# Performance work log

Hardware: AMD Instinct MI355X
Metric: run time of the kernel (lower is better)

## Reference

```python
import jax, jax.numpy as jnp
import numpy as np

K = 5        # spline kernel_size per dim (dim=2 -> 25 kernel weights)
NPG = 75     # MNIST superpixel nodes per graph


def _spline_conv(x, src, dst, pseudo, emask, W, root, bias):
    """SplineConv, dim=2, kernel_size=5, degree=1 open splines, aggr='mean'.
    emask in {0,1} masks out coalesced-away (duplicate/self-loop) edges."""
    n = x.shape[0]
    v = jnp.clip(pseudo, 0.0, 1.0) * (K - 1)
    bot = jnp.clip(jnp.floor(v), 0, K - 2)
    frac = v - bot                                   # [E,2]
    bot = bot.astype(jnp.int32)
    xj = x[src] * emask[:, None]                     # [E,Fin] gathered source feats
    # aggregate-then-transform: acc[k,i,:] = sum over edges into i with basis k
    acc = jnp.zeros((K * K, n, x.shape[1]), x.dtype)
    for o0 in (0, 1):
        for o1 in (0, 1):
            w = (frac[:, 0] if o0 else 1.0 - frac[:, 0]) * (frac[:, 1] if o1 else 1.0 - frac[:, 1])
            kk = (bot[:, 0] + o0) + K * (bot[:, 1] + o1)
            acc = acc.at[kk, dst].add(w[:, None] * xj)
    out = jnp.einsum('knf,kfo->no', acc, W)
    deg = jax.ops.segment_sum(emask, dst, num_segments=n)
    return out / jnp.maximum(deg, 1.0)[:, None] + x @ root + bias


def _pool(x, pos, valid, batch, src, dst, emask, size, G, B):
    """voxel_grid + max_pool with static shapes: S=B*G*G clusters, masked."""
    S = B * G * G
    c = jnp.clip(jnp.floor(pos / size).astype(jnp.int32), 0, G - 1)
    cl = batch * (G * G) + c[:, 1] * G + c[:, 0]
    xm = jnp.where(valid[:, None] > 0, x, -1e30)
    px = jax.ops.segment_max(xm, cl, num_segments=S)
    cnt = jax.ops.segment_sum(valid, cl, num_segments=S)
    sval = (cnt > 0).astype(x.dtype)
    px = jnp.where(sval[:, None] > 0, px, 0.0)
    ppos = jax.ops.segment_sum(pos * valid[:, None], cl, num_segments=S) / jnp.maximum(cnt, 1.0)[:, None]
    nb = jnp.arange(S, dtype=jnp.int32) // (G * G)
    # remap edges to clusters; mask self loops and duplicates (= coalesce)
    nsrc, ndst = cl[src], cl[dst]
    m = (emask > 0) & (nsrc != ndst)
    a0 = jnp.where(m, nsrc, S)
    b0 = jnp.where(m, ndst, S)
    order = jnp.lexsort((b0, a0))
    a, b = a0[order], b0[order]
    first = jnp.concatenate([jnp.array([True]), (a[1:] != a[:-1]) | (b[1:] != b[:-1])])
    keep = jnp.zeros(src.shape[0], dtype=bool).at[order].set(first & (a < S))
    kf = keep.astype(x.dtype)
    # T.Cartesian(cat=False, norm=True): pseudo = (pos_src-pos_dst)/(2*max|.|)+0.5
    cart = ppos[nsrc] - ppos[ndst]
    amax = jnp.maximum(jnp.max(jnp.abs(cart) * kf[:, None]), 1e-12)
    pseudo = cart / (2.0 * amax) + 0.5
    return px, ppos, sval, nb, nsrc, ndst, kf, pseudo


def _forward(x, pos, src, dst, W1, r1, b1, W2, r2, b2, W3, r3, b3, fw1, fb1, fw2, fb2):
    N = x.shape[0]
    B = N // NPG
    batch = jnp.arange(N, dtype=jnp.int32) // NPG
    valid = jnp.ones((N,), x.dtype)
    emask = jnp.ones((src.shape[0],), x.dtype)
    cart = pos[src] - pos[dst]
    pseudo = cart / (2.0 * jnp.maximum(jnp.max(jnp.abs(cart)), 1e-12)) + 0.5
    x = jax.nn.elu(_spline_conv(x, src, dst, pseudo, emask, W1, r1, b1))
    x, pos, valid, batch, src, dst, emask, pseudo = _pool(x, pos, valid, batch, src, dst, emask, 5.0, 6, B)
    x = jax.nn.elu(_spline_conv(x, src, dst, pseudo, emask, W2, r2, b2))
    x, pos, valid, batch, src, dst, emask, pseudo = _pool(x, pos, valid, batch, src, dst, emask, 7.0, 5, B)
    x = jax.nn.elu(_spline_conv(x, src, dst, pseudo, emask, W3, r3, b3))
    # max_pool_x(cluster, x, batch, size=4): 2x2 voxel grid (size=14, end=27.99)
    c = jnp.clip(jnp.floor(pos / 14.0).astype(jnp.int32), 0, 1)
    cl = batch * 4 + c[:, 1] * 2 + c[:, 0]
    xm = jnp.where(valid[:, None] > 0, x, -1e30)
    px = jax.ops.segment_max(xm, cl, num_segments=B * 4)
    cnt = jax.ops.segment_sum(valid, cl, num_segments=B * 4)
    px = jnp.where((cnt > 0)[:, None], px, 0.0)
    h = jax.nn.elu(px.reshape(B, 4 * 64) @ fw1.T + fb1)
    logits = h @ fw2.T + fb2  # F.dropout is identity in eval mode
    return jax.nn.log_softmax(logits, axis=1)


def setup_inputs() -> dict:
    key = jax.random.key(0)
    ks = jax.random.split(key, 16)
    B, EPG = 1024, 1392
    N = B * NPG
    x = jax.random.normal(ks[0], (N, 1), jnp.float32)
    pos = jax.random.uniform(ks[1], (N, 2), jnp.float32) * 27.99
    s = jax.random.randint(ks[2], (B, EPG), 0, NPG)
    d = (s + 1 + jax.random.randint(ks[3], (B, EPG), 0, NPG - 1)) % NPG  # no self loops
    off = (jnp.arange(B, dtype=jnp.int32) * NPG)[:, None]
    src = (s + off).reshape(-1)
    dst = (d + off).reshape(-1)
    rn = lambda k, sh, sc: jax.random.normal(k, sh, jnp.float32) * sc
    return dict(x=x, pos=pos, src=src, dst=dst,
                W1=rn(ks[4], (25, 1, 32), 0.2), r1=rn(ks[5], (1, 32), 0.2), b1=jnp.zeros((32,), jnp.float32),
                W2=rn(ks[6], (25, 32, 64), 0.05), r2=rn(ks[7], (32, 64), 0.1), b2=jnp.zeros((64,), jnp.float32),
                W3=rn(ks[8], (25, 64, 64), 0.04), r3=rn(ks[9], (64, 64), 0.08), b3=jnp.zeros((64,), jnp.float32),
                fw1=rn(ks[10], (128, 256), 0.06), fb1=jnp.zeros((128,), jnp.float32),
                fw2=rn(ks[11], (10, 128), 0.09), fb2=jnp.zeros((10,), jnp.float32))


def reference(x, pos, src, dst, W1, r1, b1, W2, r2, b2, W3, r3, b3, fw1, fb1, fw2, fb2):
    return _forward(x, pos, src, dst, W1, r1, b1, W2, r2, b2, W3, r3, b3, fw1, fb1, fw2, fb2)
```

## Files before the change

kernel.cpp:

```cpp
#include <hip/hip_runtime.h>
#include <math.h>

#define NPG 75
#define KDIM 5

typedef _Float16 half8 __attribute__((ext_vector_type(8)));
typedef float f32x4 __attribute__((ext_vector_type(4)));

__device__ __forceinline__ float eluf(float v){ return v > 0.f ? v : expf(v) - 1.f; }

__device__ __forceinline__ void atomAddF(float* p, float v){ unsafeAtomicAdd(p, v); }

__device__ __forceinline__ unsigned fenc(float f){
    unsigned u = __float_as_uint(f);
    return (u & 0x80000000u) ? ~u : (u | 0x80000000u);
}
__device__ __forceinline__ float fdec(unsigned u){
    return (u & 0x80000000u) ? __uint_as_float(u & 0x7FFFFFFFu) : __uint_as_float(~u);
}

__device__ __forceinline__ void fma25(float (&r)[25], const float (&wx)[5], const float (&wyx)[5]){
    #pragma unroll
    for (int b1 = 0; b1 < 5; b1++)
        #pragma unroll
        for (int b0 = 0; b0 < 5; b0++)
            asm("v_fmac_f32 %0, %1, %2" : "+v"(r[b1 * 5 + b0]) : "v"(wx[b0]), "v"(wyx[b1]));
}

__device__ __forceinline__ void spline2(float c0, float c1, float am, int* kks, float* wsp){
    float denom = 2.f * fmaxf(am, 1e-12f);
    float p0 = c0 / denom + 0.5f;
    float p1 = c1 / denom + 0.5f;
    p0 = fminf(fmaxf(p0, 0.f), 1.f) * 4.f;
    p1 = fminf(fmaxf(p1, 0.f), 1.f) * 4.f;
    float b0 = fminf(floorf(p0), 3.f);
    float b1 = fminf(floorf(p1), 3.f);
    float f0 = p0 - b0, f1 = p1 - b1;
    int i0 = (int)b0, i1 = (int)b1;
    wsp[0] = (1.f - f0) * (1.f - f1); kks[0] = i0     + KDIM *  i1;
    wsp[1] =        f0  * (1.f - f1); kks[1] = i0 + 1 + KDIM *  i1;
    wsp[2] = (1.f - f0) *        f1 ; kks[2] = i0     + KDIM * (i1 + 1);
    wsp[3] =        f0  *        f1 ; kks[3] = i0 + 1 + KDIM * (i1 + 1);
}

__device__ __forceinline__ void spline_pay(float2 c, float denom, float* d){
    float p0 = fminf(fmaxf(c.x / denom + 0.5f, 0.f), 1.f) * 4.f;
    float p1 = fminf(fmaxf(c.y / denom + 0.5f, 0.f), 1.f) * 4.f;
    float b0 = fminf(floorf(p0), 3.f);
    float b1 = fminf(floorf(p1), 3.f);
    int i0 = (int)b0, i1 = (int)b1;
    float f0 = p0 - b0, f1 = p1 - b1;
    #pragma unroll
    for (int k = 0; k < 4; k++){
        d[k]     = (k == i0) ? (1.f - f0) : ((k == i0 + 1) ? f0 : 0.f);
        d[4 + k] = (k == i1) ? (1.f - f1) : ((k == i1 + 1) ? f1 : 0.f);
    }
}

__global__ __launch_bounds__(256) void prep_k(
        const float* __restrict__ W2, const float* __restrict__ r2,
        const float* __restrict__ W3, const float* __restrict__ r3,
        _Float16* __restrict__ Wz2, _Float16* __restrict__ Wz3, int nW,
        const float* __restrict__ pos, const int* __restrict__ src,
        const int* __restrict__ dst, int E4, int gA, unsigned* __restrict__ outbits){
    const int blk = blockIdx.x;
    if (blk < nW){
        int gid = blk * 256 + threadIdx.x;
        const int T2 = 26 * 32 * 64;
        const int T3 = 26 * 64 * 64;
        const float* W; const float* root; _Float16* Wz; int FIN; int g;
        if (gid < T2){ W = W2; root = r2; Wz = Wz2; FIN = 32; g = gid; }
        else if (gid < T2 + T3){ W = W3; root = r3; Wz = Wz3; FIN = 64; g = gid - T2; }
        else return;
        int k = g >> 6, n = g & 63;
        float v = (k < 25 * FIN) ? W[(size_t)k * 64 + n] : root[(size_t)(k - 25 * FIN) * 64 + n];
        int kt = k >> 5, kr = k & 31, quad = kr >> 3, j = kr & 7;
        int lane = (quad << 4) | (n & 15);
        int nt = n >> 4;
        Wz[(((size_t)(kt * 4 + nt) * 64 + lane) << 3) + j] = (_Float16)v;
    } else {
        float cand = 0.f;
        for (int i = (blk - nW) * 256 + threadIdx.x; i < E4; i += gA * 256){
            int4 s4 = ((const int4*)src)[i];
            int4 d4 = ((const int4*)dst)[i];
            #pragma unroll
            for (int k = 0; k < 4; k++){
                int s = (&s4.x)[k], d = (&d4.x)[k];
                float c0 = pos[s*2]   - pos[d*2];
                float c1 = pos[s*2+1] - pos[d*2+1];
                cand = fmaxf(cand, fmaxf(fabsf(c0), fabsf(c1)));
            }
        }
        __shared__ float sm[256];
        sm[threadIdx.x] = cand; __syncthreads();
        for (int o = 128; o > 0; o >>= 1){
            if (threadIdx.x < o) sm[threadIdx.x] = fmaxf(sm[threadIdx.x], sm[threadIdx.x + o]);
            __syncthreads();
        }
        if (threadIdx.x == 0) atomicMax(outbits, __float_as_uint(sm[0]));
    }
}

__global__ __launch_bounds__(512) void conv1dedup_k(
        const float* __restrict__ x, const float* __restrict__ pos,
        const int* __restrict__ src, const int* __restrict__ dst, int EPG,
        const unsigned* __restrict__ amaxp,
        const float* __restrict__ W1, const float* __restrict__ r1, const float* __restrict__ b1,
        float* __restrict__ px1, float* __restrict__ pp1, float* __restrict__ sv1,
        int* __restrict__ easrc, float2* __restrict__ ecart,
        int* __restrict__ rowptr2, int* __restrict__ kcnt, unsigned* __restrict__ amaxbits){
    __shared__ __align__(16) float acc[NPG * 28];
    __shared__ float deg[NPG];
    __shared__ float xl[NPG], p0l[NPG], p1l[NPG];
    __shared__ int   cli[NPG];
    __shared__ float W1s[800], r1s[32], b1s[32];
    __shared__ unsigned px[36 * 32];
    __shared__ float cnt[36], ps[72], ppS[72];
    __shared__ unsigned pm[36 * 36];
    __shared__ float degs[36];
    __shared__ int rs[37], cur[36];
    __shared__ float red[8];
    __shared__ unsigned short sdS[2048];

    const int b = blockIdx.x, t = threadIdx.x;
    const int lane = t & 63, wid = t >> 6;
    const int n0 = b * NPG, e0 = b * EPG;

    const float am = __uint_as_float(*amaxp);

    for (int i = t; i < NPG * 28; i += 512) acc[i] = 0.f;
    for (int i = t; i < 36 * 32; i += 512) px[i] = 0u;
    for (int i = t; i < 36 * 36; i += 512) pm[i] = 0xFFFFFFFFu;
    if (t < NPG) deg[t] = 0.f;
    if (t < 36){ cnt[t] = 0.f; degs[t] = 0.f; }
    if (t < 72) ps[t] = 0.f;
    for (int i = t; i < 800; i += 512) W1s[i] = W1[i];
    if (t < 32){ r1s[t] = r1[t]; b1s[t] = b1[t]; }
    if (t < NPG){
        float p0 = pos[(n0 + t) * 2], p1 = pos[(n0 + t) * 2 + 1];
        xl[t] = x[n0 + t]; p0l[t] = p0; p1l[t] = p1;
        int c0 = min(max((int)floorf(p0 / 5.f), 0), 5);
        int c1 = min(max((int)floorf(p1 / 5.f), 0), 5);
        cli[t] = c1 * 6 + c0;
    }
    __syncthreads();

    if (t < NPG){
        int c = cli[t];
        atomAddF(&cnt[c], 1.f);
        atomAddF(&ps[c*2],     p0l[t]);
        atomAddF(&ps[c*2 + 1], p1l[t]);
    }
    #pragma unroll 4
    for (int it = 0; it < 4; it++){
        int e = t + it * 512;
        if (e < EPG){
            int s = src[e0 + e] - n0;
            int d = dst[e0 + e] - n0;
            sdS[e] = (unsigned short)(s | (d << 8));
            float c0 = p0l[s] - p0l[d];
            float c1 = p1l[s] - p1l[d];
            int kks[4]; float wsp[4];
            spline2(c0, c1, am, kks, wsp);
            float xv = xl[s];
            #pragma unroll
            for (int c = 0; c < 4; c++) atomAddF(&acc[d*28 + kks[c]], wsp[c] * xv);
            atomAddF(&deg[d], 1.f);
        }
    }
    __syncthreads();

    if (t < 36){
        float c = cnt[t], m = fmaxf(c, 1.f);
        float q0 = ps[t*2] / m, q1 = ps[t*2 + 1] / m;
        ppS[t*2] = q0; ppS[t*2 + 1] = q1;
        pp1[(b*36 + t)*2]     = q0;
        pp1[(b*36 + t)*2 + 1] = q1;
        sv1[b*36 + t] = (c > 0.f) ? 1.f : 0.f;
    }
    {
        const int o = t & 31;
        float wreg[25];
        #pragma unroll
        for (int k = 0; k < 25; k++) wreg[k] = W1s[k * 32 + o];
        const float rro = r1s[o], bbo = b1s[o];
        const int ii = t >> 5;
        #pragma unroll
        for (int r = 0; r < 5; r++){
            int i = ii + r * 16;
            if (i < NPG){
                const float4* ar = (const float4*)(acc + i * 28);
                float s = 0.f;
                #pragma unroll
                for (int q = 0; q < 7; q++){
                    float4 aq = ar[q];
                    s += aq.x * wreg[q*4];
                    if (q*4 + 1 < 25) s += aq.y * wreg[q*4 + 1];
                    if (q*4 + 2 < 25) s += aq.z * wreg[q*4 + 2];
                    if (q*4 + 3 < 25) s += aq.w * wreg[q*4 + 3];
                }
                float v = s / fmaxf(deg[i], 1.f) + xl[i] * rro + bbo;
                v = eluf(v);
                atomicMax(&px[cli[i]*32 + o], fenc(v));
            }
        }
    }
    int lab[4];
    #pragma unroll 4
    for (int it = 0; it < 4; it++){
        int e = t + it * 512;
        lab[it] = 0;
        if (e < EPG){
            int sd = (int)sdS[e];
            int a  = cli[sd & 255];
            int bb = cli[sd >> 8];
            lab[it] = a | (bb << 8) | ((a != bb) ? 0x10000 : 0);
            if (a != bb) atomicMin(&pm[a * 36 + bb], (unsigned)e);
        }
    }
    __syncthreads();

    for (int idx = t; idx < 36 * 32; idx += 512){
        int s_ = idx >> 5;
        px1[(size_t)(b*36)*32 + idx] = (cnt[s_] > 0.f) ? fdec(px[idx]) : 0.f;
    }
    float cand = 0.f;
    unsigned keptM = 0;
    #pragma unroll 4
    for (int it = 0; it < 4; it++){
        int e = t + it * 512;
        int L = lab[it];
        if (L & 0x10000){
            int a = L & 255, bb = (L >> 8) & 255;
            if (pm[a * 36 + bb] == (unsigned)e){
                keptM |= 1u << it;
                atomAddF(&degs[bb], 1.f);
                float c0 = ppS[a*2]     - ppS[bb*2];
                float c1 = ppS[a*2 + 1] - ppS[bb*2 + 1];
                cand = fmaxf(cand, fmaxf(fabsf(c0), fabsf(c1)));
            }
        }
    }
    #pragma unroll
    for (int o = 1; o < 64; o <<= 1) cand = fmaxf(cand, __shfl_xor(cand, o, 64));
    if (lane == 0) red[wid] = cand;
    __syncthreads();
    if (t == 0){
        float m = red[0];
        #pragma unroll
        for (int i = 1; i < 8; i++) m = fmaxf(m, red[i]);
        atomicMax(amaxbits, __float_as_uint(m));
    }
    if (t < 64){
        int v = (t < 36) ? (int)degs[t] : 0;
        int incl = v;
        #pragma unroll
        for (int o = 1; o < 64; o <<= 1){
            int u = __shfl_up(incl, o, 64);
            if (t >= o) incl += u;
        }
        if (t == 0) rs[0] = 0;
        if (t < 36) rs[t + 1] = incl;
    }
    __syncthreads();
    if (t < 36){
        rowptr2[(b*36 + t)*2]     = e0 + rs[t];
        rowptr2[(b*36 + t)*2 + 1] = e0 + rs[t + 1];
        cur[t] = rs[t];
    }
    if (t == 0) kcnt[b] = rs[36];
    __syncthreads();
    #pragma unroll 4
    for (int it = 0; it < 4; it++){
        if (keptM & (1u << it)){
            int L = lab[it];
            int a = L & 255, bb = (L >> 8) & 255;
            int slot = atomicAdd(&cur[bb], 1);
            easrc[e0 + slot] = b*36 + a;
            ecart[e0 + slot] = make_float2(ppS[a*2] - ppS[bb*2], ppS[a*2 + 1] - ppS[bb*2 + 1]);
        }
    }
}

__global__ __launch_bounds__(1024) void dedup_pool_k(
        const int* __restrict__ easrc_in, const int* __restrict__ rowptr_in,
        const int* __restrict__ kcnt_in,
        const float* __restrict__ xin,
        const float* __restrict__ pp1, const float* __restrict__ sv1,
        int EPG,
        float* __restrict__ px2, float* __restrict__ pp2, float* __restrict__ sv2,
        int* __restrict__ easrc, float2* __restrict__ ecart,
        int* __restrict__ rowptr2, int* __restrict__ kcnt, unsigned* __restrict__ amaxbits){
    constexpr int GG = 25, NN = 36;
    __shared__ unsigned pm[GG * GG];
    __shared__ float degs[GG];
    __shared__ int rs[GG + 1];
    __shared__ int cur[GG];
    __shared__ float red[16];
    __shared__ int   clS[NN];
    __shared__ int   vld[NN];
    __shared__ int   rsS[NN + 1];
    __shared__ float ppS[2 * GG];
    __shared__ unsigned px[GG * 64];
    __shared__ float cnt[GG], ps[2 * GG];
    __shared__ unsigned short abS[1280];

    const int b = blockIdx.x, t = threadIdx.x;
    const int lane = t & 63, wid = t >> 6;
    const int e0 = b * EPG;
    const int cb25 = b * GG;
    const int nb36 = b * NN;

    for (int i = t; i < GG * GG; i += 1024) pm[i] = 0xFFFFFFFFu;
    for (int i = t; i < GG * 64; i += 1024) px[i] = 0u;
    if (t < GG){ degs[t] = 0.f; cnt[t] = 0.f; }
    if (t < 2 * GG) ps[t] = 0.f;
    if (t < NN){
        float v  = sv1[nb36 + t];
        float p0 = pp1[(nb36 + t)*2], p1 = pp1[(nb36 + t)*2 + 1];
        int c0 = min(max((int)floorf(p0 / 7.f), 0), 4);
        int c1 = min(max((int)floorf(p1 / 7.f), 0), 4);
        clS[t] = c1 * 5 + c0;
        vld[t] = (v > 0.f) ? 1 : 0;
        rsS[t] = rowptr_in[(nb36 + t)*2] - e0;
    }
    if (t == 0) rsS[NN] = kcnt_in[b];
    __syncthreads();

    const int kn = rsS[NN];

    if (t < NN && vld[t]){
        int c = clS[t];
        atomAddF(&cnt[c], 1.f);
        atomAddF(&ps[c*2],     pp1[(nb36 + t)*2]);
        atomAddF(&ps[c*2 + 1], pp1[(nb36 + t)*2 + 1]);
    }
    for (int idx = t; idx < NN * 64; idx += 1024){
        int i = idx >> 6, f = idx & 63;
        if (vld[i])
            atomicMax(&px[clS[i]*64 + f], fenc(xin[(size_t)(nb36 + i)*64 + f]));
    }
    #pragma unroll 2
    for (int it = 0; it < 2; it++){
        int s = t + it * 1024;
        if (s < kn){
            int r = 0;
            while (r < NN - 1 && rsS[r + 1] <= s) r++;
            int a2 = clS[easrc_in[e0 + s] - nb36];
            int b2 = clS[r];
            abS[s] = (unsigned short)(a2 | (b2 << 8) | ((a2 != b2) ? 0x8000 : 0));
            if (a2 != b2) atomicMin(&pm[a2 * GG + b2], (unsigned)s);
        }
    }
    __syncthreads();

    if (t < GG){
        float c = cnt[t], m = fmaxf(c, 1.f);
        float q0 = ps[t*2] / m, q1 = ps[t*2 + 1] / m;
        ppS[t*2] = q0; ppS[t*2 + 1] = q1;
        pp2[(cb25 + t)*2]     = q0;
        pp2[(cb25 + t)*2 + 1] = q1;
        sv2[cb25 + t] = (c > 0.f) ? 1.f : 0.f;
    }
    for (int idx = t; idx < GG * 64; idx += 1024){
        int s_ = idx >> 6;
        px2[(size_t)cb25*64 + idx] = (cnt[s_] > 0.f) ? fdec(px[idx]) : 0.f;
    }
    __syncthreads();

    float cand = 0.f;
    #pragma unroll 2
    for (int it = 0; it < 2; it++){
        int s = t + it * 1024;
        if (s < kn){
            int A = (int)abS[s];
            if (A & 0x8000){
                int a2 = A & 255, b2 = (A >> 8) & 127;
                if (pm[a2 * GG + b2] == (unsigned)s){
                    atomAddF(&degs[b2], 1.f);
                    float c0 = ppS[a2*2]     - ppS[b2*2];
                    float c1 = ppS[a2*2 + 1] - ppS[b2*2 + 1];
                    cand = fmaxf(cand, fmaxf(fabsf(c0), fabsf(c1)));
                }
            }
        }
    }
    #pragma unroll
    for (int o = 1; o < 64; o <<= 1) cand = fmaxf(cand, __shfl_xor(cand, o, 64));
    if (lane == 0) red[wid] = cand;
    __syncthreads();
    if (t == 0){
        float m = red[0];
        #pragma unroll
        for (int i = 1; i < 16; i++) m = fmaxf(m, red[i]);
        atomicMax(amaxbits, __float_as_uint(m));
    }
    if (t < 64){
        int v = (t < GG) ? (int)degs[t] : 0;
        int incl = v;
        #pragma unroll
        for (int o = 1; o < 64; o <<= 1){
            int u = __shfl_up(incl, o, 64);
            if (t >= o) incl += u;
        }
        if (t == 0) rs[0] = 0;
        if (t < GG) rs[t + 1] = incl;
    }
    __syncthreads();
    if (t < GG){
        rowptr2[(cb25 + t)*2]     = e0 + rs[t];
        rowptr2[(cb25 + t)*2 + 1] = e0 + rs[t + 1];
        cur[t] = rs[t];
    }
    if (t == 0) kcnt[b] = rs[GG];
    __syncthreads();
    #pragma unroll 2
    for (int it = 0; it < 2; it++){
        int s = t + it * 1024;
        if (s < kn){
            int A = (int)abS[s];
            if (A & 0x8000){
                int a2 = A & 255, b2 = (A >> 8) & 127;
                if (pm[a2 * GG + b2] == (unsigned)s){
                    int slot = atomicAdd(&cur[b2], 1);
                    easrc[e0 + slot] = cb25 + a2;
                    ecart[e0 + slot] = make_float2(ppS[a2*2] - ppS[b2*2], ppS[a2*2 + 1] - ppS[b2*2 + 1]);
                }
            }
        }
    }
}

__global__ __launch_bounds__(256) void conv_gather32_k(
        const float* __restrict__ x, const int* __restrict__ easrc,
        const float2* __restrict__ ecart, const unsigned* __restrict__ amaxp,
        const int* __restrict__ rowptr2, _Float16* __restrict__ Aout){
    constexpr int FIN = 32;
    constexpr int KTOT = 26 * FIN;
    __shared__ __align__(16) float pay[4][36][8];
    __shared__ int asrcS[4][36];
    const int w = threadIdx.x >> 6, lane = threadIdx.x & 63;
    const int node = blockIdx.x * 4 + w;
    const int row0 = rowptr2[node*2], row1 = rowptr2[node*2 + 1];
    const int ne = row1 - row0;
    const int sub = lane >> 5;
    const int f = lane & (FIN - 1);

    if (lane < ne){
        float am = __uint_as_float(*amaxp);
        spline_pay(ecart[row0 + lane], 2.f * fmaxf(am, 1e-12f), &pay[w][lane][0]);
        asrcS[w][lane] = easrc[row0 + lane];
    }

    float r[25];
    #pragma unroll
    for (int b = 0; b < 25; b++) r[b] = 0.f;

    int j = sub;
    int aNext = 0;
    float xvCur = 0.f;
    if (j < ne){
        int aCur = asrcS[w][j];
        xvCur = x[(size_t)aCur * FIN + f];
        int j1 = (j + 2 < ne) ? j + 2 : j;
        aNext = asrcS[w][j1];
    }
    for (; j < ne; j += 2){
        int jN  = j + 2;
        int jNs = (jN < ne) ? jN : j;
        int jN2 = (jN + 2 < ne) ? jN + 2 : jNs;
        float xvN = x[(size_t)aNext * FIN + f];
        int aN2 = asrcS[w][jN2];
        float4 wa = *(const float4*)&pay[w][j][0];
        float4 wb = *(const float4*)&pay[w][j][4];
        float wx4 = 1.f - (wa.x + wa.y + wa.z + wa.w);
        float wy4 = 1.f - (wb.x + wb.y + wb.z + wb.w);
        float wx[5]  = {wa.x, wa.y, wa.z, wa.w, wx4};
        float wyx[5] = {wb.x * xvCur, wb.y * xvCur, wb.z * xvCur, wb.w * xvCur, wy4 * xvCur};
        fma25(r, wx, wyx);
        xvCur = xvN; aNext = aN2;
    }

    #pragma unroll
    for (int b = 0; b < 25; b++) r[b] += __shfl_xor(r[b], 32, 64);

    float inv = 1.f / (float)max(ne, 1);
    _Float16* dstrow = Aout + (size_t)node * KTOT;
    #pragma unroll
    for (int b = 0; b < 25; b++)
        if ((b & 1) == sub) dstrow[b * 32 + f] = (_Float16)(r[b] * inv);
    if (sub == 0) dstrow[25 * 32 + f] = (_Float16)x[(size_t)node * 32 + f];
}

__global__ __launch_bounds__(256) void conv_mfma832_k(
        const _Float16* __restrict__ A, const _Float16* __restrict__ Wz,
        const float* __restrict__ bias, int M, float* __restrict__ out){
    constexpr int KTOT = 832;
    constexpr int NSTEP = KTOT / 32;
    const int w = threadIdx.x >> 6, lane = threadIdx.x & 63;
    const int m0 = blockIdx.x * 64 + w * 16;
    const int quad = lane >> 4;

    f32x4 acc[4];
    #pragma unroll
    for (int nt = 0; nt < 4; nt++) acc[nt] = (f32x4){0.f, 0.f, 0.f, 0.f};

    const half8* __restrict__ Arow = (const half8*)(A + (size_t)(m0 + (lane & 15)) * KTOT);
    const half8* __restrict__ Wp   = (const half8*)Wz + lane;

    for (int kt = 0; kt < NSTEP; kt++){
        half8 a = Arow[kt * 4 + quad];
        #pragma unroll
        for (int nt = 0; nt < 4; nt++){
            half8 b = Wp[(kt * 4 + nt) * 64];
            acc[nt] = __builtin_amdgcn_mfma_f32_16x16x32_f16(a, b, acc[nt], 0, 0, 0);
        }
    }

    float* cp = out + (size_t)m0 * 64;
    const int r = quad * 4, c = lane & 15;
    #pragma unroll
    for (int nt = 0; nt < 4; nt++){
        float bv = bias[nt * 16 + c];
        #pragma unroll
        for (int i = 0; i < 4; i++)
            cp[(size_t)(r + i) * 64 + nt * 16 + c] = eluf(acc[nt][i] + bv);
    }
}

__global__ __launch_bounds__(1024) void conv3f_k(
        const float* __restrict__ x, const int* __restrict__ easrc,
        const float2* __restrict__ ecart, const unsigned* __restrict__ amaxp,
        const int* __restrict__ rowptr2, const _Float16* __restrict__ Wz,
        const float* __restrict__ bias, float* __restrict__ out){
    constexpr int PAD = 1672;
    __shared__ __align__(16) _Float16 Alds[32 * PAD];
    __shared__ __align__(16) float scratchF[3456];
    __shared__ int asrcS[16][24];

    const int w = threadIdx.x >> 6, lane = threadIdx.x & 63;
    const float am = __uint_as_float(*amaxp);
    const float denom = 2.f * fmaxf(am, 1e-12f);
    float* payW = scratchF + w * 24 * 8;

    #pragma unroll
    for (int i = 0; i < 2; i++){
        const int nloc = w * 2 + i;
        const int node = blockIdx.x * 32 + nloc;
        const int row0 = rowptr2[node*2], row1 = rowptr2[node*2 + 1];
        const int ne = row1 - row0;

        if (lane < ne){
            spline_pay(ecart[row0 + lane], denom, payW + lane * 8);
            asrcS[w][lane] = easrc[row0 + lane];
        }

        float r[25];
        #pragma unroll
        for (int b = 0; b < 25; b++) r[b] = 0.f;

        int j = 0;
        int aNext = 0;
        float xvCur = 0.f;
        if (j < ne){
            int aCur = asrcS[w][j];
            xvCur = x[(size_t)aCur * 64 + lane];
            int j1 = (1 < ne) ? 1 : 0;
            aNext = asrcS[w][j1];
        }
        for (; j < ne; j++){
            int jN  = j + 1;
            int jNs = (jN < ne) ? jN : j;
            int jN2 = (jN + 1 < ne) ? jN + 1 : jNs;
            float xvN = x[(size_t)aNext * 64 + lane];
            int aN2 = asrcS[w][jN2];
            float4 wa = *(const float4*)(payW + j * 8);
            float4 wb = *(const float4*)(payW + j * 8 + 4);
            float wx4 = 1.f - (wa.x + wa.y + wa.z + wa.w);
            float wy4 = 1.f - (wb.x + wb.y + wb.z + wb.w);
            float wx[5]  = {wa.x, wa.y, wa.z, wa.w, wx4};
            float wyx[5] = {wb.x * xvCur, wb.y * xvCur, wb.z * xvCur, wb.w * xvCur, wy4 * xvCur};
            fma25(r, wx, wyx);
            xvCur = xvN; aNext = aN2;
        }

        float inv = 1.f / (float)max(ne, 1);
        _Float16* dstrow = &Alds[nloc * PAD];
        #pragma unroll
        for (int b = 0; b < 25; b++) dstrow[b * 64 + lane] = (_Float16)(r[b] * inv);
        dstrow[25 * 64 + lane] = (_Float16)x[(size_t)node * 64 + lane];
    }
    __syncthreads();

    const int tile = w & 7, khalf = w >> 3;
    const int mt = tile >> 2, nt = tile & 3;
    const int quad = lane >> 4, mr = lane & 15;
    f32x4 acc = (f32x4){0.f, 0.f, 0.f, 0.f};
    const _Float16* arow = &Alds[(mt * 16 + mr) * PAD];
    const half8* __restrict__ Wp = (const half8*)Wz + lane;
    const int kt0 = khalf * 26;
    for (int kt = 0; kt < 26; kt++){
        half8 a = *(const half8*)(arow + (kt0 + kt) * 32 + quad * 8);
        half8 b = Wp[((kt0 + kt) * 4 + nt) * 64];
        acc = __builtin_amdgcn_mfma_f32_16x16x32_f16(a, b, acc, 0, 0, 0);
    }
    const int r_ = quad * 4, c_ = lane & 15;
    if (khalf == 1){
        float* Cp = scratchF + tile * 256;
        #pragma unroll
        for (int i = 0; i < 4; i++) Cp[(r_ + i) * 16 + c_] = acc[i];
    }
    __syncthreads();
    if (khalf == 0){
        const float* Cp = scratchF + tile * 256;
        float* cp = out + (size_t)(blockIdx.x * 32 + mt * 16) * 64;
        float bv = bias[nt * 16 + c_];
        #pragma unroll
        for (int i = 0; i < 4; i++)
            cp[(size_t)(r_ + i) * 64 + nt * 16 + c_] = eluf(acc[i] + Cp[(r_ + i) * 16 + c_] + bv);
    }
}

__global__ __launch_bounds__(256) void final_k(
        const float* __restrict__ xin, const float* __restrict__ ppin,
        const float* __restrict__ svin,
        const float* __restrict__ fw1, const float* __restrict__ fb1,
        const float* __restrict__ fw2, const float* __restrict__ fb2,
        float* __restrict__ out){
    __shared__ unsigned px[4 * 64];
    __shared__ float cnt[4];
    __shared__ int cli[25];
    __shared__ float xr[256];
    __shared__ float h[128];
    __shared__ float lg[10];
    __shared__ float lse;
    const int b = blockIdx.x, t = threadIdx.x;

    if (t < 4*64) px[t] = 0u;
    if (t < 4) cnt[t] = 0.f;
    if (t < 25){
        float v  = svin[b*25 + t];
        float p0 = ppin[(b*25 + t)*2], p1 = ppin[(b*25 + t)*2 + 1];
        int c0 = min(max((int)floorf(p0 / 14.f), 0), 1);
        int c1 = min(max((int)floorf(p1 / 14.f), 0), 1);
        int c = c1 * 2 + c0;
        cli[t] = (v > 0.f) ? c : -1;
    }
    __syncthreads();
    if (t < 25 && cli[t] >= 0) atomAddF(&cnt[cli[t]], 1.f);
    __syncthreads();
    for (int idx = t; idx < 25 * 64; idx += 256){
        int i = idx >> 6, f = idx & 63;
        if (cli[i] >= 0)
            atomicMax(&px[cli[i]*64 + f], fenc(xin[(size_t)(b*25 + i)*64 + f]));
    }
    __syncthreads();
    xr[t] = (cnt[t >> 6] > 0.f) ? fdec(px[t]) : 0.f;
    __syncthreads();
    if (t < 128){
        float s = fb1[t];
        const float4* wrow = (const float4*)(fw1 + (size_t)t * 256);
        #pragma unroll 4
        for (int i = 0; i < 64; i++){
            float4 q = wrow[i];
            s += xr[i*4]   * q.x;
            s += xr[i*4+1] * q.y;
            s += xr[i*4+2] * q.z;
            s += xr[i*4+3] * q.w;
        }
        h[t] = eluf(s);
    }
    __syncthreads();
    if (t < 10){
        float s2 = fb2[t];
        const float* w2 = fw2 + (size_t)t * 128;
        for (int j = 0; j < 128; j++) s2 += h[j] * w2[j];
        lg[t] = s2;
    }
    __syncthreads();
    if (t == 0){
        float m = lg[0];
        for (int c = 1; c < 10; c++) m = fmaxf(m, lg[c]);
        float se = 0.f;
        for (int c = 0; c < 10; c++) se += expf(lg[c] - m);
        lse = m + logf(se);
    }
    __syncthreads();
    if (t < 10) out[(size_t)b*10 + t] = lg[t] - lse;
}

extern "C" void kernel_launch(void* const* d_in, const int* in_sizes, int n_in,
                              void* d_out, int out_size, void* d_ws, size_t ws_size,
                              hipStream_t stream) {
    const float* x   = (const float*)d_in[0];
    const float* pos = (const float*)d_in[1];
    const int*   src = (const int*)d_in[2];
    const int*   dst = (const int*)d_in[3];
    const float* W1  = (const float*)d_in[4];
    const float* r1  = (const float*)d_in[5];
    const float* b1  = (const float*)d_in[6];
    const float* W2  = (const float*)d_in[7];
    const float* r2  = (const float*)d_in[8];
    const float* b2  = (const float*)d_in[9];
    const float* W3  = (const float*)d_in[10];
    const float* r3  = (const float*)d_in[11];
    const float* b3  = (const float*)d_in[12];
    const float* fw1 = (const float*)d_in[13];
    const float* fb1 = (const float*)d_in[14];
    const float* fw2 = (const float*)d_in[15];
    const float* fb2 = (const float*)d_in[16];
    float* out = (float*)d_out;

    const int N   = in_sizes[0];
    const int E   = in_sizes[2];
    const int B   = N / NPG;
    const int EPG = E / B;
    const int S1  = B * 36;
    const int S2  = B * 25;

    float* w = (float*)d_ws;
    size_t off = 0;
    auto alloc = [&](size_t nelem){ size_t o = off; off += (nelem + 63) & ~(size_t)63; return o; };

    size_t o_scal = alloc(4);
    size_t o_px1  = alloc((size_t)S1 * 32);
    size_t o_pp1  = alloc((size_t)S1 * 2);
    size_t o_sv1  = alloc(S1);
    size_t o_easrc= alloc(E);
    size_t o_ecart= alloc((size_t)2 * E);
    size_t o_kcnt = alloc(B);
    size_t o_rp2  = alloc((size_t)2 * S1);
    size_t o_rp3  = alloc((size_t)2 * S2);
    size_t o_out2 = alloc((size_t)S1 * 64);
    size_t o_px2  = alloc((size_t)S2 * 64);
    size_t o_pp2  = alloc((size_t)S2 * 2);
    size_t o_sv2  = alloc(S2);
    size_t o_out3 = alloc((size_t)S2 * 64);
    size_t o_wz2  = alloc((size_t)26 * 32 * 64 / 2 + 64);
    size_t o_wz3  = alloc((size_t)26 * 64 * 64 / 2 + 64);
    size_t o_accA = alloc(((size_t)S1 * 832 + 1) / 2);

    hipMemsetAsync(w + o_scal, 0, 4 * sizeof(float), stream);

    unsigned* scal = (unsigned*)(w + o_scal);
    _Float16* Wz2  = (_Float16*)(w + o_wz2);
    _Float16* Wz3  = (_Float16*)(w + o_wz3);
    _Float16* A16  = (_Float16*)(w + o_accA);

    const int E4 = E / 4;
    int gA = (E4 + 255) / 256; if (gA > 512) gA = 512;
    const int nW = (26 * 32 * 64 + 26 * 64 * 64 + 255) / 256;
    prep_k<<<nW + gA, 256, 0, stream>>>(W2, r2, W3, r3, Wz2, Wz3, nW,
                                        pos, src, dst, E4, gA, scal + 0);

    conv1dedup_k<<<B, 512, 0, stream>>>(x, pos, src, dst, EPG, scal + 0, W1, r1, b1,
                                        w + o_px1, w + o_pp1, w + o_sv1,
                                        (int*)(w + o_easrc), (float2*)(w + o_ecart),
                                        (int*)(w + o_rp2), (int*)(w + o_kcnt), scal + 1);

    conv_gather32_k<<<S1 / 4, 256, 0, stream>>>(
        w + o_px1, (int*)(w + o_easrc), (const float2*)(w + o_ecart), scal + 1,
        (int*)(w + o_rp2), A16);
    conv_mfma832_k<<<S1 / 64, 256, 0, stream>>>(A16, Wz2, b2, S1, w + o_out2);

    dedup_pool_k<<<B, 1024, 0, stream>>>(
        (int*)(w + o_easrc), (int*)(w + o_rp2), (int*)(w + o_kcnt),
        w + o_out2, w + o_pp1, w + o_sv1, EPG,
        w + o_px2, w + o_pp2, w + o_sv2,
        (int*)(w + o_easrc), (float2*)(w + o_ecart),
        (int*)(w + o_rp3), (int*)(w + o_kcnt), scal + 2);

    conv3f_k<<<S2 / 32, 1024, 0, stream>>>(
        w + o_px2, (int*)(w + o_easrc), (const float2*)(w + o_ecart), scal + 2,
        (int*)(w + o_rp3), Wz3, b3, w + o_out3);

    final_k<<<B, 256, 0, stream>>>(w + o_out3, w + o_pp2, w + o_sv2,
                                   fw1, fb1, fw2, fb2, out);
}
```

Measured before the change: 321.6 us.

## Fuse third spline conv with final pooling and MLP head per graph

Merges the third conv kernel and the final pool/MLP kernel into one kernel with one block per graph. Each block handles that graph's 25 clusters, padding the 32-row MFMA tile with zeroed LDS rows, keeps conv outputs in shared memory, and runs the max-pool and FC layers in place. This drops one launch and the global write and re-read of the layer-3 output. In exchange, about 22% of the MFMA rows are padding, and the block grid now has B blocks instead of S2/32.

New measurement: 320.1 us (median of 3 runs). Within noise of the previous version (-0.5%).

```diff
diff --git a/kernel.cpp b/kernel.cpp
--- a/kernel.cpp
+++ b/kernel.cpp
@@ -528,69 +528,105 @@
     }
 }
 
-__global__ __launch_bounds__(1024) void conv3f_k(
-        const float* __restrict__ x, const int* __restrict__ easrc,
-        const float2* __restrict__ ecart, const unsigned* __restrict__ amaxp,
-        const int* __restrict__ rowptr2, const _Float16* __restrict__ Wz,
-        const float* __restrict__ bias, float* __restrict__ out){
+__global__ __launch_bounds__(1024) void conv3pf_k(
+        const float* __restrict__ x,
+        const int* __restrict__ easrc, const float2* __restrict__ ecart,
+        const unsigned* __restrict__ amaxp,
+        const int* __restrict__ rowptr3,
+        const _Float16* __restrict__ Wz, const float* __restrict__ bias,
+        const float* __restrict__ pp2, const float* __restrict__ sv2,
+        const float* __restrict__ fw1, const float* __restrict__ fb1,
+        const float* __restrict__ fw2, const float* __restrict__ fb2,
+        float* __restrict__ out){
     constexpr int PAD = 1672;
     __shared__ __align__(16) _Float16 Alds[32 * PAD];
-    __shared__ __align__(16) float scratchF[3456];
+    __shared__ __align__(16) float scr[4096];
     __shared__ int asrcS[16][24];
-
-    const int w = threadIdx.x >> 6, lane = threadIdx.x & 63;
+    __shared__ unsigned px4[4 * 64];
+    __shared__ float cnt4[4];
+    __shared__ int cli25[25];
+    __shared__ float xr[256];
+    __shared__ float h[128];
+    __shared__ float lg[10];
+    __shared__ float lse;
+
+    const int b = blockIdx.x, t = threadIdx.x;
+    const int w = t >> 6, lane = t & 63;
+    const int cb25 = b * 25;
+
+    {
+        unsigned* az = (unsigned*)&Alds[25 * PAD];
+        for (int i = t; i < 7 * PAD / 2; i += 1024) az[i] = 0u;
+    }
+    if (t < 256) px4[t] = 0u;
+    if (t < 4) cnt4[t] = 0.f;
+    if (t < 25){
+        float v = sv2[cb25 + t];
+        float p0 = pp2[(cb25 + t)*2], p1 = pp2[(cb25 + t)*2 + 1];
+        int c0 = min(max((int)floorf(p0 / 14.f), 0), 1);
+        int c1 = min(max((int)floorf(p1 / 14.f), 0), 1);
+        cli25[t] = (v > 0.f) ? (c1 * 2 + c0) : -1;
+    }
+
     const float am = __uint_as_float(*amaxp);
     const float denom = 2.f * fmaxf(am, 1e-12f);
-    float* payW = scratchF + w * 24 * 8;
+    float* payW = scr + w * 192;
 
     #pragma unroll
     for (int i = 0; i < 2; i++){
         const int nloc = w * 2 + i;
-        const int node = blockIdx.x * 32 + nloc;
-        const int row0 = rowptr2[node*2], row1 = rowptr2[node*2 + 1];
-        const int ne = row1 - row0;
-
-        if (lane < ne){
-            spline_pay(ecart[row0 + lane], denom, payW + lane * 8);
-            asrcS[w][lane] = easrc[row0 + lane];
-        }
-
-        float r[25];
-        #pragma unroll
-        for (int b = 0; b < 25; b++) r[b] = 0.f;
-
-        int j = 0;
-        int aNext = 0;
-        float xvCur = 0.f;
-        if (j < ne){
-            int aCur = asrcS[w][j];
-            xvCur = x[(size_t)aCur * 64 + lane];
-            int j1 = (1 < ne) ? 1 : 0;
-            aNext = asrcS[w][j1];
-        }
-        for (; j < ne; j++){
-            int jN  = j + 1;
-            int jNs = (jN < ne) ? jN : j;
-            int jN2 = (jN + 1 < ne) ? jN + 1 : jNs;
-            float xvN = x[(size_t)aNext * 64 + lane];
-            int aN2 = asrcS[w][jN2];
-            float4 wa = *(const float4*)(payW + j * 8);
-            float4 wb = *(const float4*)(payW + j * 8 + 4);
-            float wx4 = 1.f - (wa.x + wa.y + wa.z + wa.w);
-            float wy4 = 1.f - (wb.x + wb.y + wb.z + wb.w);
-            float wx[5]  = {wa.x, wa.y, wa.z, wa.w, wx4};
-            float wyx[5] = {wb.x * xvCur, wb.y * xvCur, wb.z * xvCur, wb.w * xvCur, wy4 * xvCur};
-            fma25(r, wx, wyx);
-            xvCur = xvN; aNext = aN2;
-        }
-
-        float inv = 1.f / (float)max(ne, 1);
-        _Float16* dstrow = &Alds[nloc * PAD];
-        #pragma unroll
-        for (int b = 0; b < 25; b++) dstrow[b * 64 + lane] = (_Float16)(r[b] * inv);
-        dstrow[25 * 64 + lane] = (_Float16)x[(size_t)node * 64 + lane];
-    }
-    __syncthreads();
+        if (nloc < 25){
+            const int node = cb25 + nloc;
+            const int row0 = rowptr3[node*2], row1 = rowptr3[node*2 + 1];
+            const int ne = row1 - row0;
+
+            if (lane < ne){
+                spline_pay(ecart[row0 + lane], denom, payW + lane * 8);
+                asrcS[w][lane] = easrc[row0 + lane];
+            }
+
+            float r[25];
+            #pragma unroll
+            for (int bq = 0; bq < 25; bq++) r[bq] = 0.f;
+
+            int j = 0;
+            int aNext = 0;
+            float xvCur = 0.f;
+            if (j < ne){
+                int aCur = asrcS[w][j];
+                xvCur = x[(size_t)aCur * 64 + lane];
+                int j1 = (1 < ne) ? 1 : 0;
+                aNext = asrcS[w][j1];
+            }
+            for (; j < ne; j++){
+                int jN  = j + 1;
+                int jNs = (jN < ne) ? jN : j;
+                int jN2 = (jN + 1 < ne) ? jN + 1 : jNs;
+                float xvN = x[(size_t)aNext * 64 + lane];
+                int aN2 = asrcS[w][jN2];
+                float4 wa = *(const float4*)(payW + j * 8);
+                float4 wb = *(const float4*)(payW + j * 8 + 4);
+                float wx4 = 1.f - (wa.x + wa.y + wa.z + wa.w);
+                float wy4 = 1.f - (wb.x + wb.y + wb.z + wb.w);
+                float wx[5]  = {wa.x, wa.y, wa.z, wa.w, wx4};
+                float wyx[5] = {wb.x * xvCur, wb.y * xvCur, wb.z * xvCur, wb.w * xvCur, wy4 * xvCur};
+                fma25(r, wx, wyx);
+                xvCur = xvN; aNext = aN2;
+            }
+
+            float inv = 1.f / (float)max(ne, 1);
+            _Float16* dstrow = &Alds[nloc * PAD];
+            #pragma unroll
+            for (int bq = 0; bq < 25; bq++) dstrow[bq * 64 + lane] = (_Float16)(r[bq] * inv);
+            dstrow[25 * 64 + lane] = (_Float16)x[(size_t)node * 64 + lane];
+        }
+    }
+    __syncthreads();
+
+    if (t < 25 && cli25[t] >= 0) atomAddF(&cnt4[cli25[t]], 1.f);
+
+    float* Cpart = scr;
+    float* out3L = scr + 2048;
 
     const int tile = w & 7, khalf = w >> 3;
     const int mt = tile >> 2, nt = tile & 3;
@@ -601,61 +637,32 @@
     const int kt0 = khalf * 26;
     for (int kt = 0; kt < 26; kt++){
         half8 a = *(const half8*)(arow + (kt0 + kt) * 32 + quad * 8);
-        half8 b = Wp[((kt0 + kt) * 4 + nt) * 64];
-        acc = __builtin_amdgcn_mfma_f32_16x16x32_f16(a, b, acc, 0, 0, 0);
+        half8 bb = Wp[((kt0 + kt) * 4 + nt) * 64];
+        acc = __builtin_amdgcn_mfma_f32_16x16x32_f16(a, bb, acc, 0, 0, 0);
     }
     const int r_ = quad * 4, c_ = lane & 15;
     if (khalf == 1){
-        float* Cp = scratchF + tile * 256;
+        float* Cp = Cpart + tile * 256;
         #pragma unroll
         for (int i = 0; i < 4; i++) Cp[(r_ + i) * 16 + c_] = acc[i];
     }
     __syncthreads();
     if (khalf == 0){
-        const float* Cp = scratchF + tile * 256;
-        float* cp = out + (size_t)(blockIdx.x * 32 + mt * 16) * 64;
+        const float* Cp = Cpart + tile * 256;
         float bv = bias[nt * 16 + c_];
         #pragma unroll
         for (int i = 0; i < 4; i++)
-            cp[(size_t)(r_ + i) * 64 + nt * 16 + c_] = eluf(acc[i] + Cp[(r_ + i) * 16 + c_] + bv);
-    }
-}
-
-__global__ __launch_bounds__(256) void final_k(
-        const float* __restrict__ xin, const float* __restrict__ ppin,
-        const float* __restrict__ svin,
-        const float* __restrict__ fw1, const float* __restrict__ fb1,
-        const float* __restrict__ fw2, const float* __restrict__ fb2,
-        float* __restrict__ out){
-    __shared__ unsigned px[4 * 64];
-    __shared__ float cnt[4];
-    __shared__ int cli[25];
-    __shared__ float xr[256];
-    __shared__ float h[128];
-    __shared__ float lg[10];
-    __shared__ float lse;
-    const int b = blockIdx.x, t = threadIdx.x;
-
-    if (t < 4*64) px[t] = 0u;
-    if (t < 4) cnt[t] = 0.f;
-    if (t < 25){
-        float v  = svin[b*25 + t];
-        float p0 = ppin[(b*25 + t)*2], p1 = ppin[(b*25 + t)*2 + 1];
-        int c0 = min(max((int)floorf(p0 / 14.f), 0), 1);
-        int c1 = min(max((int)floorf(p1 / 14.f), 0), 1);
-        int c = c1 * 2 + c0;
-        cli[t] = (v > 0.f) ? c : -1;
-    }
-    __syncthreads();
-    if (t < 25 && cli[t] >= 0) atomAddF(&cnt[cli[t]], 1.f);
-    __syncthreads();
-    for (int idx = t; idx < 25 * 64; idx += 256){
+            out3L[(mt * 16 + r_ + i) * 64 + nt * 16 + c_] = eluf(acc[i] + Cp[(r_ + i) * 16 + c_] + bv);
+    }
+    __syncthreads();
+
+    for (int idx = t; idx < 25 * 64; idx += 1024){
         int i = idx >> 6, f = idx & 63;
-        if (cli[i] >= 0)
-            atomicMax(&px[cli[i]*64 + f], fenc(xin[(size_t)(b*25 + i)*64 + f]));
-    }
-    __syncthreads();
-    xr[t] = (cnt[t >> 6] > 0.f) ? fdec(px[t]) : 0.f;
+        if (cli25[i] >= 0)
+            atomicMax(&px4[cli25[i]*64 + f], fenc(out3L[i * 64 + f]));
+    }
+    __syncthreads();
+    if (t < 256) xr[t] = (cnt4[t >> 6] > 0.f) ? fdec(px4[t]) : 0.f;
     __syncthreads();
     if (t < 128){
         float s = fb1[t];
@@ -735,7 +742,6 @@
     size_t o_px2  = alloc((size_t)S2 * 64);
     size_t o_pp2  = alloc((size_t)S2 * 2);
     size_t o_sv2  = alloc(S2);
-    size_t o_out3 = alloc((size_t)S2 * 64);
     size_t o_wz2  = alloc((size_t)26 * 32 * 64 / 2 + 64);
     size_t o_wz3  = alloc((size_t)26 * 64 * 64 / 2 + 64);
     size_t o_accA = alloc(((size_t)S1 * 832 + 1) / 2);
@@ -770,10 +776,10 @@
         (int*)(w + o_easrc), (float2*)(w + o_ecart),
         (int*)(w + o_rp3), (int*)(w + o_kcnt), scal + 2);
 
-    conv3f_k<<<S2 / 32, 1024, 0, stream>>>(
-        w + o_px2, (int*)(w + o_easrc), (const float2*)(w + o_ecart), scal + 2,
-        (int*)(w + o_rp3), Wz3, b3, w + o_out3);
-
-    final_k<<<B, 256, 0, stream>>>(w + o_out3, w + o_pp2, w + o_sv2,
-                                   fw1, fb1, fw2, fb2, out);
-}
+    conv3pf_k<<<B, 1024, 0, stream>>>(
+        w + o_px2,
+        (int*)(w + o_easrc), (const float2*)(w + o_ecart), scal + 2,
+        (int*)(w + o_rp3), Wz3, b3,
+        w + o_pp2, w + o_sv2,
+        fw1, fb1, fw2, fb2, out);
+}
```
